# Optimization experiments

Hardware: AMD Instinct MI355X
Metric: run time of the kernel (lower is better)

Reference implementation:

```python
import jax, jax.numpy as jnp
import numpy as np

B, T, D_MODEL, D_STATE = 4, 4096, 1024, 256


def setup_inputs() -> dict:
    key = jax.random.key(0)
    ks = jax.random.split(key, 6)
    return {
        "x": jax.random.normal(ks[0], (B, T, D_MODEL), dtype=jnp.float32),
        "state": jnp.zeros((B, D_STATE), dtype=jnp.float32),
        "W_in": jax.random.normal(ks[1], (D_MODEL, D_STATE), dtype=jnp.float32) / np.sqrt(D_MODEL),
        "b_in": jnp.zeros((D_STATE,), dtype=jnp.float32),
        "lambda_param": jax.random.normal(ks[2], (D_STATE,), dtype=jnp.float32),
        "gamma_param": jax.random.normal(ks[3], (D_STATE,), dtype=jnp.float32),
        "W_out": jax.random.normal(ks[4], (D_STATE, D_MODEL), dtype=jnp.float32) / np.sqrt(D_STATE),
        "b_out": jnp.zeros((D_MODEL,), dtype=jnp.float32),
    }


def reference(x, state, W_in, b_in, lambda_param, gamma_param, W_out, b_out):
    # u: [B, T, d_state]
    u = jnp.einsum("btd,ds->bts", x, W_in) + b_in
    decay = jax.nn.sigmoid(lambda_param)          # [d_state]
    gu = gamma_param * u                          # [B, T, d_state]

    # linear recurrence h_t = decay * h_{t-1} + gu_t via associative scan over T
    # elements: (a, b) representing h -> a*h + b; combine: (a2*a1, a2*b1 + b2)
    a = jnp.broadcast_to(decay, gu.shape)         # [B, T, d_state]

    def combine(l, r):
        a1, b1 = l
        a2, b2 = r
        return (a2 * a1, a2 * b1 + b2)

    A, Bc = jax.lax.associative_scan(combine, (a, gu), axis=1)
    h = A * state[:, None, :] + Bc                # [B, T, d_state]

    y = jnp.einsum("bts,sd->btd", h, W_out) + b_out
    return y, h[:, -1, :]
```

## Files before the change

### kernel.cpp

```cpp
#include <hip/hip_runtime.h>
#include <hip/hip_bf16.h>
#include <math.h>

#define BB 4
#define TT 4096
#define DM 1024
#define DS 256
#define MROWS (BB*TT)

#define LCH 32
#define NCH (TT/LCH)

#define BM 128
#define BK 64

typedef __attribute__((ext_vector_type(8))) _Float16 half8v;
typedef __attribute__((ext_vector_type(4))) float float4v;

__device__ __forceinline__ float sigmoidf_dev(float x) {
    return 1.0f / (1.0f + expf(-x));
}

__device__ __forceinline__ void gload16(const void* g, void* l) {
    __builtin_amdgcn_global_load_lds(
        (const __attribute__((address_space(1))) void*)g,
        (__attribute__((address_space(3))) void*)l, 16, 0, 0);
}

__global__ __launch_bounds__(256) void cvt_weights(
    const float* __restrict__ W1, _Float16* __restrict__ T1,
    const float* __restrict__ W2, _Float16* __restrict__ T2)
{
    const int half = blockIdx.x >> 10;
    int idx = (blockIdx.x & 1023) * 256 + threadIdx.x;
    const float* W = half ? W2 : W1;
    _Float16* T = half ? T2 : T1;
    const int K = half ? DS : DM;
    const int N = half ? DM : DS;
    int n = idx / K, k = idx - n * K;
    T[idx] = (_Float16)W[(size_t)k * N + n];
}

__global__ __launch_bounds__(256) void cvt_x(
    const float* __restrict__ x, _Float16* __restrict__ xf)
{
    size_t u = (size_t)blockIdx.x * 256 + threadIdx.x;
    const float* p = x + u * 8;
    float4 a = *(const float4*)p;
    float4 b = *(const float4*)(p + 4);
    half8v h;
    h[0] = (_Float16)a.x; h[1] = (_Float16)a.y; h[2] = (_Float16)a.z; h[3] = (_Float16)a.w;
    h[4] = (_Float16)b.x; h[5] = (_Float16)b.y; h[6] = (_Float16)b.z; h[7] = (_Float16)b.w;
    *(half8v*)(xf + u * 8) = h;
}

template<int BN, bool FUSE>
__global__ __launch_bounds__(256) void gemm_f16(
    const _Float16* __restrict__ A, const _Float16* __restrict__ Bt,
    float* __restrict__ C, int M, int N, int K, int GN,
    const float* __restrict__ bias, const float* __restrict__ scale,
    const float* __restrict__ lam, float* __restrict__ csum)
{
    constexpr int WCOLS = BN / 2;
    constexpr int NF    = WCOLS / 16;
    constexpr int ABYTES = BM * BK * 2;
    constexpr int BBYTES = BN * BK * 2;
    constexpr int BUFB   = ABYTES + BBYTES;
    constexpr int SMSZ   = (2 * BUFB > 34816) ? 2 * BUFB : 34816;
    __shared__ char smem[SMSZ];

    const int nwg = gridDim.x;
    const int bid = blockIdx.x;
    const int wgid = (bid & 7) * (nwg >> 3) + (bid >> 3);
    const int bm = wgid / GN;
    const int bn = wgid - bm * GN;

    const int tid  = threadIdx.x;
    const int lane = tid & 63;
    const int wv   = tid >> 6;
    const int wr   = wv >> 1;
    const int wc   = wv & 1;
    const int lrow = lane & 15;
    const int q16  = lane >> 4;

    const int NT = K / BK;
    float4v acc[4][NF] = {};

#define STAGE(T, Q)                                                               \
    do {                                                                          \
        const int k0_ = (T) * BK;                                                 \
        char* base_ = smem + (Q) * BUFB;                                          \
        _Pragma("unroll")                                                         \
        for (int p = 0; p < 4; p++) {                                             \
            int c = tid + p * 256, r = c >> 3, chp = c & 7;                       \
            const _Float16* g = A + (size_t)(bm * BM + r) * K + k0_               \
                                  + ((chp ^ (r & 7)) << 3);                       \
            gload16(g, base_ + c * 16);                                           \
        }                                                                         \
        _Pragma("unroll")                                                         \
        for (int p = 0; p < BN / 32; p++) {                                       \
            int c = tid + p * 256, r = c >> 3, chp = c & 7;                       \
            const _Float16* g = Bt + (size_t)(bn * BN + r) * K + k0_              \
                                   + ((chp ^ (r & 7)) << 3);                      \
            gload16(g, base_ + ABYTES + c * 16);                                  \
        }                                                                         \
    } while (0)

    STAGE(0, 0);
    __syncthreads();

    for (int t = 0; t < NT; ++t) {
        const int Q = t & 1;
        if (t + 1 < NT) STAGE(t + 1, Q ^ 1);

        char* const rb = smem + Q * BUFB;

        half8v a[4][2], b[NF][2];
#pragma unroll
        for (int i = 0; i < 4; i++) {
            int row = wr * 64 + i * 16 + lrow;
#pragma unroll
            for (int ss = 0; ss < 2; ss++) {
                int ch = ss * 4 + q16;
                a[i][ss] = *(const half8v*)(rb + ((row * 8 + (ch ^ (row & 7))) << 4));
            }
        }
#pragma unroll
        for (int j = 0; j < NF; j++) {
            int row = wc * WCOLS + j * 16 + lrow;
#pragma unroll
            for (int ss = 0; ss < 2; ss++) {
                int ch = ss * 4 + q16;
                b[j][ss] = *(const half8v*)(rb + ABYTES + ((row * 8 + (ch ^ (row & 7))) << 4));
            }
        }

#pragma unroll
        for (int ss = 0; ss < 2; ss++)
#pragma unroll
            for (int i = 0; i < 4; i++)
#pragma unroll
                for (int j = 0; j < NF; j++)
                    acc[i][j] = __builtin_amdgcn_mfma_f32_16x16x32_f16(a[i][ss], b[j][ss], acc[i][j], 0, 0, 0);

        __syncthreads();
    }

    float* gul = (float*)smem;
#pragma unroll
    for (int j = 0; j < NF; j++) {
        int col = bn * BN + wc * WCOLS + j * 16 + lrow;
        float bi = bias[col];
        float sc = scale ? scale[col] : 1.0f;
#pragma unroll
        for (int i = 0; i < 4; i++) {
            int r0 = bm * BM + wr * 64 + i * 16 + q16 * 4;
#pragma unroll
            for (int reg = 0; reg < 4; reg++) {
                float v = (acc[i][j][reg] + bi) * sc;
                C[(size_t)(r0 + reg) * N + col] = v;
                if constexpr (FUSE) {
                    int lr = wr * 64 + i * 16 + q16 * 4 + reg;
                    int lc = wc * WCOLS + j * 16 + lrow;
                    gul[lr * 68 + lc] = v;
                }
            }
        }
    }

    if constexpr (FUSE) {
        __syncthreads();
        const int lc = tid >> 6;
        const int ch = tid & 63;
        const int gcol = bn * BN + ch;
        const float d = sigmoidf_dev(lam[gcol]);
        float h = 0.0f;
#pragma unroll
        for (int rr = 0; rr < LCH; rr++)
            h = fmaf(d, h, gul[(lc * LCH + rr) * 68 + ch]);
        const int row0 = bm * BM;
        const int b    = row0 >> 12;
        const int gch  = ((row0 & 4095) >> 5) + lc;
        csum[((size_t)b * NCH + gch) * DS + gcol] = h;
    }
#undef STAGE
}

__global__ __launch_bounds__(256) void carry_scan(
    const float* __restrict__ csum, const float* __restrict__ state,
    const float* __restrict__ lam, float* __restrict__ carry, float* __restrict__ hlast)
{
    const int s = threadIdx.x;
    const int b = blockIdx.x;
    const float d = sigmoidf_dev(lam[s]);
    float dL = d;
#pragma unroll
    for (int i = 0; i < 5; i++) dL *= dL;
    float H = state[(size_t)b * DS + s];
#pragma unroll 8
    for (int k = 0; k < NCH; k++) {
        carry[((size_t)b * NCH + k) * DS + s] = H;
        H = fmaf(dL, H, csum[((size_t)b * NCH + k) * DS + s]);
    }
    hlast[(size_t)b * DS + s] = H;
}

__global__ __launch_bounds__(256) void scan_final(
    const float* __restrict__ gu, const float* __restrict__ lam,
    const float* __restrict__ carry, _Float16* __restrict__ hf)
{
    const int s = threadIdx.x;
    const int chunk = blockIdx.x;
    const int b = blockIdx.y;
    const float d = sigmoidf_dev(lam[s]);
    const size_t base = ((size_t)b * TT + (size_t)chunk * LCH) * DS + s;
    const float* p = gu + base;
    _Float16* ph = hf + base;
    float h = carry[((size_t)b * NCH + chunk) * DS + s];
#pragma unroll
    for (int t = 0; t < LCH; t++) {
        h = fmaf(d, h, p[(size_t)t * DS]);
        ph[(size_t)t * DS] = (_Float16)h;
    }
}

extern "C" void kernel_launch(void* const* d_in, const int* in_sizes, int n_in,
                              void* d_out, int out_size, void* d_ws, size_t ws_size,
                              hipStream_t stream) {
    const float* x     = (const float*)d_in[0];
    const float* state = (const float*)d_in[1];
    const float* W_in  = (const float*)d_in[2];
    const float* b_in  = (const float*)d_in[3];
    const float* lam   = (const float*)d_in[4];
    const float* gamma = (const float*)d_in[5];
    const float* W_out = (const float*)d_in[6];
    const float* b_out = (const float*)d_in[7];

    float* y     = (float*)d_out;
    float* hlast = y + (size_t)MROWS * DM;

    char* ws = (char*)d_ws;
    const size_t MB = 1024 * 1024;
    float*     gu    = (float*)(ws);
    float*     csum  = (float*)(ws + 16 * MB);
    float*     carry = (float*)(ws + 16 * MB + 512 * 1024);
    _Float16*  hf    = (_Float16*)(ws + 17 * MB);
    _Float16*  w1t   = (_Float16*)(ws + 25 * MB);
    _Float16*  w2t   = (_Float16*)(ws + 25 * MB + 512 * 1024);
    _Float16*  xf    = (_Float16*)(ws + 26 * MB);

    cvt_weights<<<dim3(2048), dim3(256), 0, stream>>>(W_in, w1t, W_out, w2t);
    cvt_x<<<dim3((MROWS * DM) / (256 * 8)), dim3(256), 0, stream>>>(x, xf);

    gemm_f16<64, true><<<dim3((MROWS / BM) * (DS / 64)), dim3(256), 0, stream>>>(
        xf, w1t, gu, MROWS, DS, DM, DS / 64, b_in, gamma, lam, csum);

    carry_scan<<<dim3(BB), dim3(256), 0, stream>>>(csum, state, lam, carry, hlast);
    scan_final<<<dim3(NCH, BB), dim3(256), 0, stream>>>(gu, lam, carry, hf);

    gemm_f16<128, false><<<dim3((MROWS / BM) * (DM / 128)), dim3(256), 0, stream>>>(
        hf, w2t, y, MROWS, DM, DS, DM / 128, b_out, nullptr, nullptr, nullptr);
}
```

Measured before the change: 74.44 us.

## Fuse fp32-to-fp16 conversion of x into first GEMM load path

Drops the separate cvt_x kernel. The first GEMM now streams fp32 x tiles straight into LDS with BK=32 and converts them to fp16 in registers with packed round-toward-zero conversion before the MFMA. This avoids writing and re-reading a 32 MB half-precision copy of x. In exchange, the GEMM reads twice the bytes per A tile, uses a smaller K step (more iterations and barriers), and rounds toward zero instead of to nearest.

```diff
diff --git a/kernel.cpp b/kernel.cpp
--- a/kernel.cpp
+++ b/kernel.cpp
@@ -12,13 +12,20 @@
 #define NCH (TT/LCH)
 
 #define BM 128
-#define BK 64
 
 typedef __attribute__((ext_vector_type(8))) _Float16 half8v;
+typedef __attribute__((ext_vector_type(2))) _Float16 half2v;
 typedef __attribute__((ext_vector_type(4))) float float4v;
 
 __device__ __forceinline__ float sigmoidf_dev(float x) {
     return 1.0f / (1.0f + expf(-x));
+}
+
+__device__ __forceinline__ half2v cvt2_rtz(float a, float b) {
+    auto r = __builtin_amdgcn_cvt_pkrtz(a, b);
+    union { decltype(r) i; half2v o; } cv;
+    cv.i = r;
+    return cv.o;
 }
 
 __device__ __forceinline__ void gload16(const void* g, void* l) {
@@ -41,37 +48,20 @@
     T[idx] = (_Float16)W[(size_t)k * N + n];
 }
 
-__global__ __launch_bounds__(256) void cvt_x(
-    const float* __restrict__ x, _Float16* __restrict__ xf)
-{
-    size_t u = (size_t)blockIdx.x * 256 + threadIdx.x;
-    const float* p = x + u * 8;
-    float4 a = *(const float4*)p;
-    float4 b = *(const float4*)(p + 4);
-    half8v h;
-    h[0] = (_Float16)a.x; h[1] = (_Float16)a.y; h[2] = (_Float16)a.z; h[3] = (_Float16)a.w;
-    h[4] = (_Float16)b.x; h[5] = (_Float16)b.y; h[6] = (_Float16)b.z; h[7] = (_Float16)b.w;
-    *(half8v*)(xf + u * 8) = h;
-}
-
-template<int BN, bool FUSE>
-__global__ __launch_bounds__(256) void gemm_f16(
-    const _Float16* __restrict__ A, const _Float16* __restrict__ Bt,
-    float* __restrict__ C, int M, int N, int K, int GN,
+__global__ __launch_bounds__(256) void gemm1_fused(
+    const float* __restrict__ x, const _Float16* __restrict__ Bt,
+    float* __restrict__ gu,
     const float* __restrict__ bias, const float* __restrict__ scale,
     const float* __restrict__ lam, float* __restrict__ csum)
 {
-    constexpr int WCOLS = BN / 2;
-    constexpr int NF    = WCOLS / 16;
-    constexpr int ABYTES = BM * BK * 2;
-    constexpr int BBYTES = BN * BK * 2;
-    constexpr int BUFB   = ABYTES + BBYTES;
-    constexpr int SMSZ   = (2 * BUFB > 34816) ? 2 * BUFB : 34816;
-    __shared__ char smem[SMSZ];
+    __shared__ char smem[40960];
+    constexpr int K = DM;
+    constexpr int BN = 64, BK = 32, NF = 2, WCOLS = 32;
 
     const int nwg = gridDim.x;
     const int bid = blockIdx.x;
     const int wgid = (bid & 7) * (nwg >> 3) + (bid >> 3);
+    const int GN = DS / BN;
     const int bm = wgid / GN;
     const int bn = wgid - bm * GN;
 
@@ -86,7 +76,126 @@
     const int NT = K / BK;
     float4v acc[4][NF] = {};
 
-#define STAGE(T, Q)                                                               \
+#define STAGE1(T, Q)                                                              \
+    do {                                                                          \
+        const int k0_ = (T) * BK;                                                 \
+        _Pragma("unroll")                                                         \
+        for (int p = 0; p < 4; p++) {                                             \
+            int c = tid + p * 256, r = c >> 3, chp = c & 7;                       \
+            const float* g = x + (size_t)(bm * BM + r) * K + k0_                  \
+                               + ((chp ^ (r & 7)) << 2);                          \
+            gload16(g, smem + (Q) * 16384 + c * 16);                              \
+        }                                                                         \
+        {                                                                         \
+            int c = tid, r = c >> 2, chp = c & 3;                                 \
+            const _Float16* g = Bt + (size_t)(bn * BN + r) * K + k0_              \
+                                   + ((chp ^ ((r >> 1) & 3)) << 3);               \
+            gload16(g, smem + 32768 + (Q) * 4096 + c * 16);                       \
+        }                                                                         \
+    } while (0)
+
+    STAGE1(0, 0);
+    __syncthreads();
+
+    for (int t = 0; t < NT; ++t) {
+        const int Q = t & 1;
+        if (t + 1 < NT) STAGE1(t + 1, Q ^ 1);
+
+        union { half2v h2[4]; half8v h8; } a[4];
+        half8v b[NF];
+#pragma unroll
+        for (int i = 0; i < 4; i++) {
+            int row = wr * 64 + i * 16 + lrow;
+            const char* ab = smem + Q * 16384 + row * 128;
+            int s = row & 7;
+            float4 fa = *(const float4*)(ab + (((2 * q16)     ^ s) << 4));
+            float4 fb = *(const float4*)(ab + (((2 * q16 + 1) ^ s) << 4));
+            a[i].h2[0] = cvt2_rtz(fa.x, fa.y);
+            a[i].h2[1] = cvt2_rtz(fa.z, fa.w);
+            a[i].h2[2] = cvt2_rtz(fb.x, fb.y);
+            a[i].h2[3] = cvt2_rtz(fb.z, fb.w);
+        }
+#pragma unroll
+        for (int j = 0; j < NF; j++) {
+            int row = wc * WCOLS + j * 16 + lrow;
+            b[j] = *(const half8v*)(smem + 32768 + Q * 4096 +
+                                    ((row * 4 + (q16 ^ ((row >> 1) & 3))) << 4));
+        }
+
+#pragma unroll
+        for (int i = 0; i < 4; i++)
+#pragma unroll
+            for (int j = 0; j < NF; j++)
+                acc[i][j] = __builtin_amdgcn_mfma_f32_16x16x32_f16(a[i].h8, b[j], acc[i][j], 0, 0, 0);
+
+        __syncthreads();
+    }
+
+    float* gul = (float*)smem;
+#pragma unroll
+    for (int j = 0; j < NF; j++) {
+        int col = bn * BN + wc * WCOLS + j * 16 + lrow;
+        float bi = bias[col];
+        float sc = scale[col];
+#pragma unroll
+        for (int i = 0; i < 4; i++) {
+            int r0 = bm * BM + wr * 64 + i * 16 + q16 * 4;
+#pragma unroll
+            for (int reg = 0; reg < 4; reg++) {
+                float v = (acc[i][j][reg] + bi) * sc;
+                gu[(size_t)(r0 + reg) * DS + col] = v;
+                int lr = wr * 64 + i * 16 + q16 * 4 + reg;
+                int lc = wc * WCOLS + j * 16 + lrow;
+                gul[lr * 68 + lc] = v;
+            }
+        }
+    }
+
+    __syncthreads();
+    const int lc = tid >> 6;
+    const int ch = tid & 63;
+    const int gcol = bn * BN + ch;
+    const float d = sigmoidf_dev(lam[gcol]);
+    float h = 0.0f;
+#pragma unroll
+    for (int rr = 0; rr < LCH; rr++)
+        h = fmaf(d, h, gul[(lc * LCH + rr) * 68 + ch]);
+    const int row0 = bm * BM;
+    const int b    = row0 >> 12;
+    const int gch  = ((row0 & 4095) >> 5) + lc;
+    csum[((size_t)b * NCH + gch) * DS + gcol] = h;
+#undef STAGE1
+}
+
+__global__ __launch_bounds__(256) void gemm2_f16(
+    const _Float16* __restrict__ A, const _Float16* __restrict__ Bt,
+    float* __restrict__ C, const float* __restrict__ bias)
+{
+    constexpr int BN = 128, BK = 64, NF = 4, WCOLS = 64;
+    constexpr int K = DS;
+    constexpr int ABYTES = BM * BK * 2;
+    constexpr int BUFB = ABYTES + BN * BK * 2;
+    __shared__ char smem[2 * BUFB];
+
+    const int nwg = gridDim.x;
+    const int bid = blockIdx.x;
+    const int wgid = (bid & 7) * (nwg >> 3) + (bid >> 3);
+    const int GN = DM / BN;
+    const int bm = wgid / GN;
+    const int bn = wgid - bm * GN;
+
+    const int tid  = threadIdx.x;
+    const int lane = tid & 63;
+    const int wv   = tid >> 6;
+    const int wr   = wv >> 1;
+    const int wc   = wv & 1;
+    const int lrow = lane & 15;
+    const int q16  = lane >> 4;
+
+    const int NT = K / BK;
+    float4v acc[4][NF] = {};
+
+#define STAGE2(T, Q)                                                              \
     do {                                                                          \
         const int k0_ = (T) * BK;                                                 \
         char* base_ = smem + (Q) * BUFB;                                          \
@@ -98,7 +207,7 @@
             gload16(g, base_ + c * 16);                                           \
         }                                                                         \
         _Pragma("unroll")                                                         \
-        for (int p = 0; p < BN / 32; p++) {                                       \
+        for (int p = 0; p < 4; p++) {                                             \
             int c = tid + p * 256, r = c >> 3, chp = c & 7;                       \
             const _Float16* g = Bt + (size_t)(bn * BN + r) * K + k0_              \
                                    + ((chp ^ (r & 7)) << 3);                      \
@@ -106,15 +215,14 @@
         }                                                                         \
     } while (0)
 
-    STAGE(0, 0);
+    STAGE2(0, 0);
     __syncthreads();
 
     for (int t = 0; t < NT; ++t) {
         const int Q = t & 1;
-        if (t + 1 < NT) STAGE(t + 1, Q ^ 1);
+        if (t + 1 < NT) STAGE2(t + 1, Q ^ 1);
 
         char* const rb = smem + Q * BUFB;
-
         half8v a[4][2], b[NF][2];
 #pragma unroll
         for (int i = 0; i < 4; i++) {
@@ -146,44 +254,19 @@
         __syncthreads();
     }
 
-    float* gul = (float*)smem;
 #pragma unroll
     for (int j = 0; j < NF; j++) {
         int col = bn * BN + wc * WCOLS + j * 16 + lrow;
         float bi = bias[col];
-        float sc = scale ? scale[col] : 1.0f;
 #pragma unroll
         for (int i = 0; i < 4; i++) {
             int r0 = bm * BM + wr * 64 + i * 16 + q16 * 4;
 #pragma unroll
-            for (int reg = 0; reg < 4; reg++) {
-                float v = (acc[i][j][reg] + bi) * sc;
-                C[(size_t)(r0 + reg) * N + col] = v;
-                if constexpr (FUSE) {
-                    int lr = wr * 64 + i * 16 + q16 * 4 + reg;
-                    int lc = wc * WCOLS + j * 16 + lrow;
-                    gul[lr * 68 + lc] = v;
-                }
-            }
-        }
-    }
-
-    if constexpr (FUSE) {
-        __syncthreads();
-        const int lc = tid >> 6;
-        const int ch = tid & 63;
-        const int gcol = bn * BN + ch;
-        const float d = sigmoidf_dev(lam[gcol]);
-        float h = 0.0f;
-#pragma unroll
-        for (int rr = 0; rr < LCH; rr++)
-            h = fmaf(d, h, gul[(lc * LCH + rr) * 68 + ch]);
-        const int row0 = bm * BM;
-        const int b    = row0 >> 12;
-        const int gch  = ((row0 & 4095) >> 5) + lc;
-        csum[((size_t)b * NCH + gch) * DS + gcol] = h;
-    }
-#undef STAGE
+            for (int reg = 0; reg < 4; reg++)
+                C[(size_t)(r0 + reg) * DM + col] = acc[i][j][reg] + bi;
+        }
+    }
+#undef STAGE2
 }
 
 __global__ __launch_bounds__(256) void carry_scan(
@@ -247,17 +330,15 @@
     _Float16*  hf    = (_Float16*)(ws + 17 * MB);
     _Float16*  w1t   = (_Float16*)(ws + 25 * MB);
     _Float16*  w2t   = (_Float16*)(ws + 25 * MB + 512 * 1024);
-    _Float16*  xf    = (_Float16*)(ws + 26 * MB);
 
     cvt_weights<<<dim3(2048), dim3(256), 0, stream>>>(W_in, w1t, W_out, w2t);
-    cvt_x<<<dim3((MROWS * DM) / (256 * 8)), dim3(256), 0, stream>>>(x, xf);
-
-    gemm_f16<64, true><<<dim3((MROWS / BM) * (DS / 64)), dim3(256), 0, stream>>>(
-        xf, w1t, gu, MROWS, DS, DM, DS / 64, b_in, gamma, lam, csum);
+
+    gemm1_fused<<<dim3((MROWS / BM) * (DS / 64)), dim3(256), 0, stream>>>(
+        x, w1t, gu, b_in, gamma, lam, csum);
 
     carry_scan<<<dim3(BB), dim3(256), 0, stream>>>(csum, state, lam, carry, hlast);
     scan_final<<<dim3(NCH, BB), dim3(256), 0, stream>>>(gu, lam, carry, hf);
 
-    gemm_f16<128, false><<<dim3((MROWS / BM) * (DM / 128)), dim3(256), 0, stream>>>(
-        hf, w2t, y, MROWS, DM, DS, DM / 128, b_out, nullptr, nullptr, nullptr);
-}
+    gemm2_f16<<<dim3((MROWS / BM) * (DM / 128)), dim3(256), 0, stream>>>(
+        hf, w2t, y, b_out);
+}
```

Result: no change. 75.11 us (+0.9%).
